# Performance work log

Measured on AMD Instinct MI355X. Metric: run time of the kernel, lower is better.

The kernel has to match this reference:

```python
import jax, jax.numpy as jnp
import numpy as np

H, C, R, L = 4, 32, 4, 2   # heads, per-head dim, num_relations, num_layers
D = H * C                  # hidden_channels = in_channels = 128
EPS_BN = 1e-5
NEG_SLOPE = 0.2


def _forward(x0, src0, dst0, ea0, src1, dst1, ea1,
             Wl, Wr, bl, br, att, conv_b,
             bn_g, bn_b, bn_m, bn_v,
             skip_W, skip_b,
             proj_W, proj_b, pbn_g, pbn_b, pbn_m, pbn_v, prelu_a,
             n_t0, n_t1):
    x = x0
    layers = [(src0, dst0, ea0, n_t0), (src1, dst1, ea1, n_t1)]
    for i, (src, dst, ea, nt) in enumerate(layers):
        xt = x[:nt]                               # [nt, D] target nodes
        out = xt @ skip_W[i] + skip_b[i]          # skip connection
        for j in range(R):                        # per-relation GATv2 + BN (eval)
            mask = (ea == j)
            xl = (x @ Wl[i, j] + bl[i, j]).reshape(-1, H, C)   # [N, H, C]
            xr = (xt @ Wr[i, j] + br[i, j]).reshape(-1, H, C)  # [nt, H, C]
            msg = xl[src] + xr[dst]                            # [E, H, C]
            logit = jnp.sum(jax.nn.leaky_relu(msg, NEG_SLOPE) * att[i, j], axis=-1)  # [E, H]
            logit = jnp.where(mask[:, None], logit, -1e9)      # mask other relations
            amax = jax.ops.segment_max(logit, dst, num_segments=nt)                  # [nt, H]
            p = jnp.exp(logit - amax[dst]) * mask[:, None]
            denom = jax.ops.segment_sum(p, dst, num_segments=nt)
            alpha = p / jnp.maximum(denom, 1e-16)[dst]                               # [E, H]
            agg = jax.ops.segment_sum(alpha[..., None] * xl[src], dst, num_segments=nt)
            agg = agg.reshape(nt, D) + conv_b[i, j]
            out = out + (agg - bn_m[i, j]) * jax.lax.rsqrt(bn_v[i, j] + EPS_BN) * bn_g[i, j] + bn_b[i, j]
        x = jax.nn.elu(out)   # dropout is identity in eval mode
    # projection head: Linear -> BN(eval) -> PReLU -> Dropout(identity)
    h = x @ proj_W + proj_b
    h = (h - pbn_m) * jax.lax.rsqrt(pbn_v + EPS_BN) * pbn_g + pbn_b
    proj = jnp.where(h > 0, h, prelu_a * h)
    return x, proj


def setup_inputs() -> dict:
    key = jax.random.key(0)
    ks = jax.random.split(key, 32)
    N0, E0, N1, E1, N2 = 100000, 400000, 30000, 150000, 8000

    def w(k, shape, s=0.1):
        return jax.random.normal(k, shape, dtype=jnp.float32) * s

    return {
        'x0': jax.random.normal(ks[0], (N0, D), dtype=jnp.float32),
        'src0': jax.random.randint(ks[1], (E0,), 0, N0),
        'dst0': jax.random.randint(ks[2], (E0,), 0, N1),
        'ea0': jax.random.randint(ks[3], (E0,), 0, R),
        'src1': jax.random.randint(ks[4], (E1,), 0, N1),
        'dst1': jax.random.randint(ks[5], (E1,), 0, N2),
        'ea1': jax.random.randint(ks[6], (E1,), 0, R),
        'Wl': w(ks[7], (L, R, D, D)), 'Wr': w(ks[8], (L, R, D, D)),
        'bl': w(ks[9], (L, R, D)), 'br': w(ks[10], (L, R, D)),
        'att': w(ks[11], (L, R, H, C)), 'conv_b': w(ks[12], (L, R, D)),
        'bn_g': 1.0 + w(ks[13], (L, R, D)), 'bn_b': w(ks[14], (L, R, D)),
        'bn_m': w(ks[15], (L, R, D)),
        'bn_v': 0.5 + jax.random.uniform(ks[16], (L, R, D), dtype=jnp.float32),
        'skip_W': w(ks[17], (L, D, D)), 'skip_b': w(ks[18], (L, D)),
        'proj_W': w(ks[19], (D, D)), 'proj_b': w(ks[20], (D,)),
        'pbn_g': 1.0 + w(ks[21], (D,)), 'pbn_b': w(ks[22], (D,)),
        'pbn_m': w(ks[23], (D,)),
        'pbn_v': 0.5 + jax.random.uniform(ks[24], (D,), dtype=jnp.float32),
        'prelu_a': jnp.full((1,), 0.25, dtype=jnp.float32),
        'n_t0': N1, 'n_t1': N2,
    }


def reference(x0, src0, dst0, ea0, src1, dst1, ea1,
              Wl, Wr, bl, br, att, conv_b,
              bn_g, bn_b, bn_m, bn_v,
              skip_W, skip_b,
              proj_W, proj_b, pbn_g, pbn_b, pbn_m, pbn_v, prelu_a,
              n_t0, n_t1):
    return _forward(x0, src0, dst0, ea0, src1, dst1, ea1,
                    Wl, Wr, bl, br, att, conv_b,
                    bn_g, bn_b, bn_m, bn_v,
                    skip_W, skip_b,
                    proj_W, proj_b, pbn_g, pbn_b, pbn_m, pbn_v, prelu_a,
                    n_t0, n_t1)
```

## Files before the change

### kernel.cpp

```cpp
#include <hip/hip_runtime.h>
#include <stdint.h>

typedef short bf16x8 __attribute__((ext_vector_type(8)));
typedef float f32x4 __attribute__((ext_vector_type(4)));

constexpr float cEPS = 1e-5f;
constexpr float cSLOPE = 0.2f;

__device__ __forceinline__ unsigned short f2b(float f){
  unsigned u = __float_as_uint(f);
  u = (u + 0x7fffu + ((u >> 16) & 1u)) >> 16;
  return (unsigned short)u;
}
__device__ __forceinline__ float b2f(unsigned short b){
  return __uint_as_float(((unsigned)b) << 16);
}

__global__ void k_f32_to_bf16(const float* __restrict__ in, unsigned short* __restrict__ out, int n8){
  int i = blockIdx.x * 256 + threadIdx.x;
  if(i >= n8) return;
  float4 v0 = ((const float4*)in)[i*2];
  float4 v1 = ((const float4*)in)[i*2 + 1];
  bf16x8 o = { (short)f2b(v0.x), (short)f2b(v0.y), (short)f2b(v0.z), (short)f2b(v0.w),
               (short)f2b(v1.x), (short)f2b(v1.y), (short)f2b(v1.z), (short)f2b(v1.w) };
  ((bf16x8*)out)[i] = o;
}

__global__ void k_build_wt(const float* __restrict__ Wl, const float* __restrict__ Wr,
                           const float* __restrict__ skW, const float* __restrict__ pjW,
                           unsigned short* __restrict__ wt){
  int idx = blockIdx.x * 256 + threadIdx.x;
  if(idx >= 19 * 16384) return;
  int mat = idx >> 14, r = idx & 16383;
  int n = r >> 7, k = r & 127;
  const float* src;
  if(mat < 8)       src = Wl + mat * 16384;
  else if(mat < 16) src = Wr + (mat - 8) * 16384;
  else if(mat < 18) src = skW + (mat - 16) * 16384;
  else              src = pjW;
  wt[idx] = f2b(src[k * 128 + n]);
}

__global__ void k_hist_key(const int* __restrict__ dst, const int* __restrict__ ea,
                           unsigned int* __restrict__ cnt, int E){
  int i = blockIdx.x * 256 + threadIdx.x;
  if(i < E) atomicAdd(cnt + (dst[i]*4 + ea[i]), 1u);
}

__device__ __forceinline__ unsigned wave_iscan(unsigned v, int lane){
  #pragma unroll
  for(int ofs = 1; ofs < 64; ofs <<= 1){
    unsigned y = __shfl_up(v, ofs);
    if(lane >= ofs) v += y;
  }
  return v;
}

__global__ __launch_bounds__(256) void k_scan_partial(
    const unsigned int* __restrict__ cnt, unsigned int* __restrict__ off,
    unsigned int* __restrict__ bsum, int n){
  __shared__ unsigned int buf[4096];
  __shared__ unsigned int wofs[4];
  const int base = blockIdx.x * 4096;
  for(int i = threadIdx.x; i < 4096; i += 256){
    int idx = base + i;
    buf[i] = (idx < n) ? cnt[idx] : 0u;
  }
  __syncthreads();
  const int lane = threadIdx.x & 63, wid = threadIdx.x >> 6;
  const int b = threadIdx.x * 16;
  unsigned loc[16]; unsigned s = 0;
  #pragma unroll
  for(int i = 0; i < 16; ++i){ loc[i] = s; s += buf[b + i]; }
  unsigned isc = wave_iscan(s, lane);
  unsigned texc = isc - s;
  if(lane == 63) wofs[wid] = isc;
  __syncthreads();
  unsigned wbase = 0;
  for(int w = 0; w < wid; ++w) wbase += wofs[w];
  unsigned tbase = wbase + texc;
  #pragma unroll
  for(int i = 0; i < 16; ++i){
    int idx = base + b + i;
    if(idx < n) off[idx] = tbase + loc[i];
  }
  if(threadIdx.x == 255) bsum[blockIdx.x] = wbase + isc;
}

__global__ void k_scan_bsum(unsigned int* __restrict__ bsum, unsigned int* __restrict__ off,
                            int nblk, int n){
  if(threadIdx.x == 0 && blockIdx.x == 0){
    unsigned acc = 0;
    for(int i = 0; i < nblk; ++i){ unsigned v = bsum[i]; bsum[i] = acc; acc += v; }
    off[n] = acc;
  }
}

__global__ void k_scan_add(unsigned int* __restrict__ off, unsigned int* __restrict__ cur,
                           const unsigned int* __restrict__ bsum, int n){
  int i = blockIdx.x * 256 + threadIdx.x;
  if(i < n){
    unsigned v = off[i] + bsum[i >> 12];
    off[i] = v;
    cur[i] = v;
  }
}

__global__ void k_scatter_key(const int* __restrict__ dst, const int* __restrict__ ea,
                              const int* __restrict__ src,
                              unsigned int* __restrict__ cursor,
                              int* __restrict__ psrc, int E){
  int i = blockIdx.x * 256 + threadIdx.x;
  if(i < E){
    unsigned int pos = atomicAdd(cursor + (dst[i]*4 + ea[i]), 1u);
    psrc[pos] = src[i];
  }
}

template<bool OUT_BF16>
__global__ __launch_bounds__(256) void k_gemm(
    const unsigned short* __restrict__ A, int M,
    const unsigned short* __restrict__ wtBase, long wtStride,
    const float* __restrict__ biasBase, int biasStride,
    void* __restrict__ outBase, long outStride)
{
  __shared__ unsigned short lw[128 * 136];
  const unsigned short* Wt = wtBase + (long)blockIdx.y * wtStride;
  #pragma unroll
  for(int it = 0; it < 8; ++it){
    int idx = it * 256 + threadIdx.x;
    int row = idx >> 4, c8 = idx & 15;
    bf16x8 v = *(const bf16x8*)(Wt + row * 128 + c8 * 8);
    *(bf16x8*)(lw + row * 136 + c8 * 8) = v;
  }

  const float* bias = biasBase + (long)blockIdx.y * biasStride;
  const int wave = threadIdx.x >> 6, lane = threadIdx.x & 63;
  const int l16 = lane & 15, lhi = lane >> 4;

  const int row0 = blockIdx.x * 64 + wave * 16;
  const int arow = row0 + l16;
  const bf16x8 zf = {0,0,0,0,0,0,0,0};
  bf16x8 afr[4];
  if(arow < M){
    #pragma unroll
    for(int kb = 0; kb < 4; ++kb)
      afr[kb] = *(const bf16x8*)(A + (long)arow*128 + kb*32 + lhi*8);
  } else {
    #pragma unroll
    for(int kb = 0; kb < 4; ++kb) afr[kb] = zf;
  }
  __syncthreads();

  const f32x4 z4 = {0.f,0.f,0.f,0.f};
  f32x4 acc[8];
  #pragma unroll
  for(int cb = 0; cb < 8; ++cb) acc[cb] = z4;
  #pragma unroll
  for(int cb = 0; cb < 8; ++cb){
    #pragma unroll
    for(int kb = 0; kb < 4; ++kb){
      bf16x8 bfr = *(const bf16x8*)(lw + (cb*16 + l16)*136 + kb*32 + lhi*8);
      acc[cb] = __builtin_amdgcn_mfma_f32_16x16x32_bf16(afr[kb], bfr, acc[cb], 0, 0, 0);
    }
  }

  #pragma unroll
  for(int cb = 0; cb < 8; ++cb){
    int col = cb*16 + l16;
    float bv = bias[col];
    #pragma unroll
    for(int q = 0; q < 4; ++q){
      int rrow = row0 + lhi*4 + q;
      if(rrow < M){
        float v = acc[cb][q] + bv;
        long oidx = (long)blockIdx.y * outStride + (long)rrow * 128 + col;
        if(OUT_BF16) ((unsigned short*)outBase)[oidx] = f2b(v);
        else         ((float*)outBase)[oidx] = v;
      }
    }
  }
}

__global__ __launch_bounds__(64) void k_dst_agg(
    const unsigned int* __restrict__ off, const int* __restrict__ psrc,
    const unsigned short* __restrict__ xl, const unsigned short* __restrict__ xr,
    const float* __restrict__ att,
    const float* __restrict__ conv_b, const float* __restrict__ bn_g, const float* __restrict__ bn_b,
    const float* __restrict__ bn_m, const float* __restrict__ bn_v,
    float* __restrict__ out, int N, int nt)
{
  const int t = blockIdx.x;
  const int lane = threadIdx.x;
  const int sub  = lane >> 4;
  const int l16  = lane & 15;

  float4 o0 = ((const float4*)(out + (long)t*128 + l16*8))[0];
  float4 o1 = ((const float4*)(out + (long)t*128 + l16*8))[1];
  float oc[8] = {o0.x,o0.y,o0.z,o0.w,o1.x,o1.y,o1.z,o1.w};

  for(int r = 0; r < 4; ++r){
    const bf16x8 xrv = *(const bf16x8*)(xr + ((long)r*nt + t)*128 + l16*8);
    const float4 a0 = ((const float4*)(att + r*128 + l16*8))[0];
    const float4 a1 = ((const float4*)(att + r*128 + l16*8))[1];
    const float av[8] = {a0.x,a0.y,a0.z,a0.w,a1.x,a1.y,a1.z,a1.w};
    float xrf[8];
    #pragma unroll
    for(int q = 0; q < 8; ++q) xrf[q] = b2f((unsigned short)xrv[q]);

    const unsigned s0 = off[t*4 + r], s1 = off[t*4 + r + 1];

    float m = -3.0e38f, den = 0.f;
    float acc[8];
    #pragma unroll
    for(int q = 0; q < 8; ++q) acc[q] = 0.f;

    for(unsigned e = s0 + sub; e < s1; e += 4){
      int s = psrc[e];
      bf16x8 xlv = *(const bf16x8*)(xl + ((long)r*N + s)*128 + l16*8);
      float xlf[8];
      #pragma unroll
      for(int q = 0; q < 8; ++q) xlf[q] = b2f((unsigned short)xlv[q]);
      float part = 0.f;
      #pragma unroll
      for(int q = 0; q < 8; ++q){
        float v = xlf[q] + xrf[q];
        v = v >= 0.f ? v : cSLOPE * v;
        part += v * av[q];
      }
      part += __shfl_xor(part, 1);
      part += __shfl_xor(part, 2);
      float nm = fmaxf(m, part);
      float corr = __expf(m - nm);
      float p = __expf(part - nm);
      den = den * corr + p;
      #pragma unroll
      for(int q = 0; q < 8; ++q) acc[q] = acc[q] * corr + p * xlf[q];
      m = nm;
    }

    #pragma unroll
    for(int ofs = 16; ofs <= 32; ofs <<= 1){
      float m2 = __shfl_xor(m, ofs);
      float d2 = __shfl_xor(den, ofs);
      float M = fmaxf(m, m2);
      float sA = __expf(m - M), sB = __expf(m2 - M);
      den = den * sA + d2 * sB;
      #pragma unroll
      for(int q = 0; q < 8; ++q){
        float a2 = __shfl_xor(acc[q], ofs);
        acc[q] = acc[q] * sA + a2 * sB;
      }
      m = M;
    }

    const float inv = 1.f / fmaxf(den, 1e-16f);
    const float4 cb0 = ((const float4*)(conv_b + r*128 + l16*8))[0];
    const float4 cb1 = ((const float4*)(conv_b + r*128 + l16*8))[1];
    const float4 gg0 = ((const float4*)(bn_g  + r*128 + l16*8))[0];
    const float4 gg1 = ((const float4*)(bn_g  + r*128 + l16*8))[1];
    const float4 bb0 = ((const float4*)(bn_b  + r*128 + l16*8))[0];
    const float4 bb1 = ((const float4*)(bn_b  + r*128 + l16*8))[1];
    const float4 mm0 = ((const float4*)(bn_m  + r*128 + l16*8))[0];
    const float4 mm1 = ((const float4*)(bn_m  + r*128 + l16*8))[1];
    const float4 vv0 = ((const float4*)(bn_v  + r*128 + l16*8))[0];
    const float4 vv1 = ((const float4*)(bn_v  + r*128 + l16*8))[1];
    const float cbv[8] = {cb0.x,cb0.y,cb0.z,cb0.w,cb1.x,cb1.y,cb1.z,cb1.w};
    const float ggv[8] = {gg0.x,gg0.y,gg0.z,gg0.w,gg1.x,gg1.y,gg1.z,gg1.w};
    const float bbv[8] = {bb0.x,bb0.y,bb0.z,bb0.w,bb1.x,bb1.y,bb1.z,bb1.w};
    const float mmv[8] = {mm0.x,mm0.y,mm0.z,mm0.w,mm1.x,mm1.y,mm1.z,mm1.w};
    const float vvv[8] = {vv0.x,vv0.y,vv0.z,vv0.w,vv1.x,vv1.y,vv1.z,vv1.w};
    #pragma unroll
    for(int q = 0; q < 8; ++q)
      oc[q] += (acc[q] * inv + cbv[q] - mmv[q]) * rsqrtf(vvv[q] + cEPS) * ggv[q] + bbv[q];
  }

  if(sub == 0){
    float4 w0 = {oc[0],oc[1],oc[2],oc[3]}, w1 = {oc[4],oc[5],oc[6],oc[7]};
    ((float4*)(out + (long)t*128 + l16*8))[0] = w0;
    ((float4*)(out + (long)t*128 + l16*8))[1] = w1;
  }
}

__global__ void k_elu_act(const float* __restrict__ in, unsigned short* __restrict__ outBf,
                          float* __restrict__ outF32, int n4){
  int i = blockIdx.x * 256 + threadIdx.x;
  if(i >= n4) return;
  float4 v = ((const float4*)in)[i];
  float4 e;
  e.x = v.x > 0.f ? v.x : __expf(v.x) - 1.f;
  e.y = v.y > 0.f ? v.y : __expf(v.y) - 1.f;
  e.z = v.z > 0.f ? v.z : __expf(v.z) - 1.f;
  e.w = v.w > 0.f ? v.w : __expf(v.w) - 1.f;
  ushort4 o = { f2b(e.x), f2b(e.y), f2b(e.z), f2b(e.w) };
  ((ushort4*)outBf)[i] = o;
  if(outF32) ((float4*)outF32)[i] = e;
}

__global__ void k_pbn_prelu(float* __restrict__ hbuf, const float* __restrict__ g, const float* __restrict__ b,
                            const float* __restrict__ m, const float* __restrict__ v,
                            const float* __restrict__ a, int n4){
  int i = blockIdx.x * 256 + threadIdx.x;
  if(i >= n4) return;
  int c4 = i & 31;
  float4 x  = ((const float4*)hbuf)[i];
  float4 gg = ((const float4*)g)[c4], bb = ((const float4*)b)[c4];
  float4 mm = ((const float4*)m)[c4], vv = ((const float4*)v)[c4];
  float al = a[0];
  float4 y;
  y.x = (x.x - mm.x) * rsqrtf(vv.x + cEPS) * gg.x + bb.x; y.x = y.x > 0.f ? y.x : al * y.x;
  y.y = (x.y - mm.y) * rsqrtf(vv.y + cEPS) * gg.y + bb.y; y.y = y.y > 0.f ? y.y : al * y.y;
  y.z = (x.z - mm.z) * rsqrtf(vv.z + cEPS) * gg.z + bb.z; y.z = y.z > 0.f ? y.z : al * y.z;
  y.w = (x.w - mm.w) * rsqrtf(vv.w + cEPS) * gg.w + bb.w; y.w = y.w > 0.f ? y.w : al * y.w;
  ((float4*)hbuf)[i] = y;
}

extern "C" void kernel_launch(void* const* d_in, const int* in_sizes, int n_in,
                              void* d_out, int out_size, void* d_ws, size_t ws_size,
                              hipStream_t stream)
{
  const float* x0     = (const float*)d_in[0];
  const int*   src0   = (const int*)d_in[1];
  const int*   dst0   = (const int*)d_in[2];
  const int*   ea0    = (const int*)d_in[3];
  const int*   src1   = (const int*)d_in[4];
  const int*   dst1   = (const int*)d_in[5];
  const int*   ea1    = (const int*)d_in[6];
  const float* Wl     = (const float*)d_in[7];
  const float* Wr     = (const float*)d_in[8];
  const float* bl     = (const float*)d_in[9];
  const float* br     = (const float*)d_in[10];
  const float* att    = (const float*)d_in[11];
  const float* conv_b = (const float*)d_in[12];
  const float* bn_g   = (const float*)d_in[13];
  const float* bn_b   = (const float*)d_in[14];
  const float* bn_m   = (const float*)d_in[15];
  const float* bn_v   = (const float*)d_in[16];
  const float* skip_W = (const float*)d_in[17];
  const float* skip_b = (const float*)d_in[18];
  const float* proj_W = (const float*)d_in[19];
  const float* proj_b = (const float*)d_in[20];
  const float* pbn_g  = (const float*)d_in[21];
  const float* pbn_b  = (const float*)d_in[22];
  const float* pbn_m  = (const float*)d_in[23];
  const float* pbn_v  = (const float*)d_in[24];
  const float* prelu_a= (const float*)d_in[25];

  const int N0 = in_sizes[0] / 128;
  const int E0 = in_sizes[1];
  const int E1 = in_sizes[4];
  const int N1 = 30000;
  const int N2 = 8000;
  const int jc = 4;

  auto al = [](size_t x){ return (x + 255) & ~(size_t)255; };
  char* p = (char*)d_ws;
  auto carve = [&](size_t bytes){ char* r = p; p += al(bytes); return r; };
  unsigned short* wt    = (unsigned short*)carve((size_t)19*16384*2);
  unsigned short* xbf   = (unsigned short*)carve((size_t)N0*256);
  unsigned short* xlb   = (unsigned short*)carve((size_t)jc*N0*256);
  unsigned short* xrb   = (unsigned short*)carve((size_t)jc*N1*256);
  unsigned int*   cnt   = (unsigned int*)carve((size_t)(N1*4+1)*4);
  unsigned int*   off   = (unsigned int*)carve((size_t)(N1*4+1)*4);
  unsigned int*   cur   = (unsigned int*)carve((size_t)(N1*4+1)*4);
  unsigned int*   bsum  = (unsigned int*)carve((size_t)256*4);
  int*            psrc  = (int*)carve((size_t)E0*4);
  float*          out1  = (float*)carve((size_t)N1*512);

  k_f32_to_bf16<<<(N0*16 + 255)/256, 256, 0, stream>>>(x0, xbf, N0*16);
  k_build_wt<<<(19*16384 + 255)/256, 256, 0, stream>>>(Wl, Wr, skip_W, proj_W, wt);

  auto run_layer = [&](int li, int N, int nt, const int* src, const int* dst, const int* ea, int E){
    const int nbins = nt * 4;
    const int nblk = (nbins + 4095) / 4096;
    hipMemsetAsync(cnt, 0, (size_t)(nbins + 1) * 4, stream);
    k_hist_key<<<(E + 255)/256, 256, 0, stream>>>(dst, ea, cnt, E);
    k_scan_partial<<<nblk, 256, 0, stream>>>(cnt, off, bsum, nbins);
    k_scan_bsum<<<1, 64, 0, stream>>>(bsum, off, nblk, nbins);
    k_scan_add<<<(nbins + 255)/256, 256, 0, stream>>>(off, cur, bsum, nbins);
    k_scatter_key<<<(E + 255)/256, 256, 0, stream>>>(dst, ea, src, cur, psrc, E);

    k_gemm<false><<<dim3((nt+63)/64, 1), 256, 0, stream>>>(
        xbf, nt, wt + (16+li)*16384, 0, skip_b + li*128, 0, out1, 0);
    k_gemm<true><<<dim3((N+63)/64, jc), 256, 0, stream>>>(
        xbf, N,  wt + (li*4)*16384,   16384, bl + (li*4)*128, 128, xlb, (long)N*128);
    k_gemm<true><<<dim3((nt+63)/64, jc), 256, 0, stream>>>(
        xbf, nt, wt + (8+li*4)*16384, 16384, br + (li*4)*128, 128, xrb, (long)nt*128);
    k_dst_agg<<<nt, 64, 0, stream>>>(
        off, psrc, xlb, xrb, att + li*512,
        conv_b + li*512, bn_g + li*512, bn_b + li*512, bn_m + li*512, bn_v + li*512,
        out1, N, nt);
  };

  run_layer(0, N0, N1, src0, dst0, ea0, E0);
  k_elu_act<<<(N1*32 + 255)/256, 256, 0, stream>>>(out1, xbf, nullptr, N1*32);
  run_layer(1, N1, N2, src1, dst1, ea1, E1);

  float* outX = (float*)d_out;
  float* outP = (float*)d_out + (size_t)N2*128;
  k_elu_act<<<(N2*32 + 255)/256, 256, 0, stream>>>(out1, xbf, outX, N2*32);
  k_gemm<false><<<dim3((N2+63)/64, 1), 256, 0, stream>>>(
      xbf, N2, wt + 18*16384, 0, proj_b, 0, outP, 0);
  k_pbn_prelu<<<(N2*32 + 255)/256, 256, 0, stream>>>(outP, pbn_g, pbn_b, pbn_m, pbn_v, prelu_a, N2*32);
}
```

Baseline: 486.7 us.

## Process the four relations in parallel warps and use lazy softmax rescaling

```diff
diff --git a/kernel.cpp b/kernel.cpp
--- a/kernel.cpp
+++ b/kernel.cpp
@@ -182,7 +182,7 @@
   }
 }
 
-__global__ __launch_bounds__(64) void k_dst_agg(
+__global__ __launch_bounds__(256) void k_dst_agg(
     const unsigned int* __restrict__ off, const int* __restrict__ psrc,
     const unsigned short* __restrict__ xl, const unsigned short* __restrict__ xr,
     const float* __restrict__ att,
@@ -190,95 +190,91 @@
     const float* __restrict__ bn_m, const float* __restrict__ bn_v,
     float* __restrict__ out, int N, int nt)
 {
+  __shared__ float contrib[4][128];
   const int t = blockIdx.x;
-  const int lane = threadIdx.x;
+  const int r = threadIdx.x >> 6;
+  const int lane = threadIdx.x & 63;
   const int sub  = lane >> 4;
   const int l16  = lane & 15;
 
-  float4 o0 = ((const float4*)(out + (long)t*128 + l16*8))[0];
-  float4 o1 = ((const float4*)(out + (long)t*128 + l16*8))[1];
-  float oc[8] = {o0.x,o0.y,o0.z,o0.w,o1.x,o1.y,o1.z,o1.w};
-
-  for(int r = 0; r < 4; ++r){
-    const bf16x8 xrv = *(const bf16x8*)(xr + ((long)r*nt + t)*128 + l16*8);
-    const float4 a0 = ((const float4*)(att + r*128 + l16*8))[0];
-    const float4 a1 = ((const float4*)(att + r*128 + l16*8))[1];
-    const float av[8] = {a0.x,a0.y,a0.z,a0.w,a1.x,a1.y,a1.z,a1.w};
-    float xrf[8];
-    #pragma unroll
-    for(int q = 0; q < 8; ++q) xrf[q] = b2f((unsigned short)xrv[q]);
-
-    const unsigned s0 = off[t*4 + r], s1 = off[t*4 + r + 1];
-
-    float m = -3.0e38f, den = 0.f;
-    float acc[8];
-    #pragma unroll
-    for(int q = 0; q < 8; ++q) acc[q] = 0.f;
-
-    for(unsigned e = s0 + sub; e < s1; e += 4){
-      int s = psrc[e];
-      bf16x8 xlv = *(const bf16x8*)(xl + ((long)r*N + s)*128 + l16*8);
-      float xlf[8];
+  const bf16x8 xrv = *(const bf16x8*)(xr + ((long)r*nt + t)*128 + l16*8);
+  float xrf[8];
+  #pragma unroll
+  for(int q = 0; q < 8; ++q) xrf[q] = b2f((unsigned short)xrv[q]);
+  const float4 a0 = ((const float4*)(att + r*128 + l16*8))[0];
+  const float4 a1 = ((const float4*)(att + r*128 + l16*8))[1];
+  const float av[8] = {a0.x,a0.y,a0.z,a0.w,a1.x,a1.y,a1.z,a1.w};
+
+  const unsigned s0 = off[t*4 + r], s1 = off[t*4 + r + 1];
+
+  float m = -3.0e38f, den = 0.f;
+  float acc[8];
+  #pragma unroll
+  for(int q = 0; q < 8; ++q) acc[q] = 0.f;
+
+  for(unsigned e = s0 + sub; e < s1; e += 4){
+    int s = psrc[e];
+    bf16x8 xlv = *(const bf16x8*)(xl + ((long)r*N + s)*128 + l16*8);
+    float xlf[8];
+    #pragma unroll
+    for(int q = 0; q < 8; ++q) xlf[q] = b2f((unsigned short)xlv[q]);
+    float part = 0.f;
+    #pragma unroll
+    for(int q = 0; q < 8; ++q){
+      float v = xlf[q] + xrf[q];
+      v = v >= 0.f ? v : cSLOPE * v;
+      part += v * av[q];
+    }
+    part += __shfl_xor(part, 1);
+    part += __shfl_xor(part, 2);
+    float p;
+    if(part > m + 8.f){
+      float corr = __expf(m - part);
+      den *= corr;
       #pragma unroll
-      for(int q = 0; q < 8; ++q) xlf[q] = b2f((unsigned short)xlv[q]);
-      float part = 0.f;
-      #pragma unroll
-      for(int q = 0; q < 8; ++q){
-        float v = xlf[q] + xrf[q];
-        v = v >= 0.f ? v : cSLOPE * v;
-        part += v * av[q];
-      }
-      part += __shfl_xor(part, 1);
-      part += __shfl_xor(part, 2);
-      float nm = fmaxf(m, part);
-      float corr = __expf(m - nm);
-      float p = __expf(part - nm);
-      den = den * corr + p;
-      #pragma unroll
-      for(int q = 0; q < 8; ++q) acc[q] = acc[q] * corr + p * xlf[q];
-      m = nm;
-    }
-
-    #pragma unroll
-    for(int ofs = 16; ofs <= 32; ofs <<= 1){
-      float m2 = __shfl_xor(m, ofs);
-      float d2 = __shfl_xor(den, ofs);
-      float M = fmaxf(m, m2);
-      float sA = __expf(m - M), sB = __expf(m2 - M);
-      den = den * sA + d2 * sB;
-      #pragma unroll
-      for(int q = 0; q < 8; ++q){
-        float a2 = __shfl_xor(acc[q], ofs);
-        acc[q] = acc[q] * sA + a2 * sB;
-      }
-      m = M;
-    }
-
+      for(int q = 0; q < 8; ++q) acc[q] *= corr;
+      m = part;
+      p = 1.f;
+    } else {
+      p = __expf(part - m);
+    }
+    den += p;
+    #pragma unroll
+    for(int q = 0; q < 8; ++q) acc[q] += p * xlf[q];
+  }
+
+  #pragma unroll
+  for(int ofs = 16; ofs <= 32; ofs <<= 1){
+    float m2 = __shfl_xor(m, ofs);
+    float d2 = __shfl_xor(den, ofs);
+    float M = fmaxf(m, m2);
+    float sA = __expf(m - M), sB = __expf(m2 - M);
+    den = den * sA + d2 * sB;
+    #pragma unroll
+    for(int q = 0; q < 8; ++q){
+      float a2 = __shfl_xor(acc[q], ofs);
+      acc[q] = acc[q] * sA + a2 * sB;
+    }
+    m = M;
+  }
+
+  if(sub == 0){
     const float inv = 1.f / fmaxf(den, 1e-16f);
-    const float4 cb0 = ((const float4*)(conv_b + r*128 + l16*8))[0];
-    const float4 cb1 = ((const float4*)(conv_b + r*128 + l16*8))[1];
-    const float4 gg0 = ((const float4*)(bn_g  + r*128 + l16*8))[0];
-    const float4 gg1 = ((const float4*)(bn_g  + r*128 + l16*8))[1];
-    const float4 bb0 = ((const float4*)(bn_b  + r*128 + l16*8))[0];
-    const float4 bb1 = ((const float4*)(bn_b  + r*128 + l16*8))[1];
-    const float4 mm0 = ((const float4*)(bn_m  + r*128 + l16*8))[0];
-    const float4 mm1 = ((const float4*)(bn_m  + r*128 + l16*8))[1];
-    const float4 vv0 = ((const float4*)(bn_v  + r*128 + l16*8))[0];
-    const float4 vv1 = ((const float4*)(bn_v  + r*128 + l16*8))[1];
-    const float cbv[8] = {cb0.x,cb0.y,cb0.z,cb0.w,cb1.x,cb1.y,cb1.z,cb1.w};
-    const float ggv[8] = {gg0.x,gg0.y,gg0.z,gg0.w,gg1.x,gg1.y,gg1.z,gg1.w};
-    const float bbv[8] = {bb0.x,bb0.y,bb0.z,bb0.w,bb1.x,bb1.y,bb1.z,bb1.w};
-    const float mmv[8] = {mm0.x,mm0.y,mm0.z,mm0.w,mm1.x,mm1.y,mm1.z,mm1.w};
-    const float vvv[8] = {vv0.x,vv0.y,vv0.z,vv0.w,vv1.x,vv1.y,vv1.z,vv1.w};
-    #pragma unroll
-    for(int q = 0; q < 8; ++q)
-      oc[q] += (acc[q] * inv + cbv[q] - mmv[q]) * rsqrtf(vvv[q] + cEPS) * ggv[q] + bbv[q];
-  }
-
-  if(sub == 0){
-    float4 w0 = {oc[0],oc[1],oc[2],oc[3]}, w1 = {oc[4],oc[5],oc[6],oc[7]};
-    ((float4*)(out + (long)t*128 + l16*8))[0] = w0;
-    ((float4*)(out + (long)t*128 + l16*8))[1] = w1;
+    #pragma unroll
+    for(int q = 0; q < 8; ++q){
+      int c = l16*8 + q;
+      float cb = conv_b[r*128 + c], gg = bn_g[r*128 + c], bb = bn_b[r*128 + c];
+      float mm = bn_m[r*128 + c],  vv = bn_v[r*128 + c];
+      contrib[r][c] = (acc[q] * inv + cb - mm) * rsqrtf(vv + cEPS) * gg + bb;
+    }
+  }
+  __syncthreads();
+  if(threadIdx.x < 64){
+    int c = threadIdx.x * 2;
+    float2 o = *(float2*)(out + (long)t*128 + c);
+    o.x += contrib[0][c]   + contrib[1][c]   + contrib[2][c]   + contrib[3][c];
+    o.y += contrib[0][c+1] + contrib[1][c+1] + contrib[2][c+1] + contrib[3][c+1];
+    *(float2*)(out + (long)t*128 + c) = o;
   }
 }
 
@@ -386,7 +382,7 @@
         xbf, N,  wt + (li*4)*16384,   16384, bl + (li*4)*128, 128, xlb, (long)N*128);
     k_gemm<true><<<dim3((nt+63)/64, jc), 256, 0, stream>>>(
         xbf, nt, wt + (8+li*4)*16384, 16384, br + (li*4)*128, 128, xrb, (long)nt*128);
-    k_dst_agg<<<nt, 64, 0, stream>>>(
+    k_dst_agg<<<nt, 256, 0, stream>>>(
         off, psrc, xlb, xrb, att + li*512,
         conv_b + li*512, bn_g + li*512, bn_b + li*512, bn_m + li*512, bn_v + li*512,
         out1, N, nt);
```

After: 478.0 us. About the same (-1.8%).
